# Kernel tuning notes

Measured on AMD Instinct MI355X. Metric: run time of the kernel, lower is better.

The kernel has to match this reference:

```python
import jax, jax.numpy as jnp
import numpy as np

K = 100          # sliding window (even: matches torch pad (K//2, K//2-1) producing T windows)
EPS = 1e-12      # added to std, per original code


def setup_inputs() -> dict:
    key = jax.random.key(0)
    x = jax.random.normal(key, (8, 16384, 128), dtype=jnp.float32)  # B x T x D
    return {"x": x}


def _sliding_mean_std(x):
    """Per-frame sliding mean/std (unbiased, ddof=1) over a reflect-padded
    window of size K, via prefix sums: O(T) instead of O(T*K)."""
    B, T, D = x.shape
    # reflect pad the time axis: left K//2, right K//2-1 -> T + K - 1 frames
    xp = jnp.pad(x, ((0, 0), (K // 2, K // 2 - 1), (0, 0)), mode="reflect")
    zero = jnp.zeros((B, 1, D), dtype=x.dtype)
    cs = jnp.concatenate([zero, jnp.cumsum(xp, axis=1)], axis=1)        # (B, T+K, D)
    cs2 = jnp.concatenate([zero, jnp.cumsum(xp * xp, axis=1)], axis=1)  # (B, T+K, D)
    s = cs[:, K:K + T] - cs[:, 0:T]    # window sums,   (B, T, D)
    s2 = cs2[:, K:K + T] - cs2[:, 0:T]  # window sumsq, (B, T, D)
    m = s / K
    var = (s2 - K * m * m) / (K - 1)    # unbiased variance (torch.std default)
    std = jnp.sqrt(jnp.maximum(var, 0.0))
    return m, std


def reference(x) -> jnp.ndarray:
    # with_mean=True, with_std=True branch of MovingAvgNorm (T >= kernel_size)
    m, std = _sliding_mean_std(x)
    return (x - m) / (std + EPS)
```

## Files before the change

### kernel.cpp

```cpp
#include <hip/hip_runtime.h>

constexpr int KWIN = 100;
constexpr int HK   = 50;
constexpr int TSUB = 64;
constexpr int MB   = 8;
constexpr int PB   = 25;

template <bool REFLECT>
__device__ __forceinline__ int tidx(int t) {
    if constexpr (REFLECT) {
        constexpr int T = 16384;
        t = (t < 0) ? -t : t;
        return (t >= T) ? (2 * T - 2 - t) : t;
    }
    return t;
}

template <bool REFLECT>
__device__ __forceinline__ void run_chunk(
    const float* __restrict__ xb, float* __restrict__ ob, const int t0)
{
    float ring[HK];
    float sx = 0.f, sq = 0.f;

    {
        float la[PB], lb[PB];
        #pragma unroll
        for (int j = 0; j < PB; ++j)
            la[j] = xb[(size_t)tidx<REFLECT>(t0 - HK + j) * 128];
        #pragma unroll
        for (int j = 0; j < PB; ++j)
            lb[j] = xb[(size_t)tidx<REFLECT>(t0 - PB + j) * 128];
        #pragma unroll
        for (int j = 0; j < PB; ++j) { sx += la[j]; sq = fmaf(la[j], la[j], sq); }
        #pragma unroll
        for (int j = 0; j < PB; ++j)
            ring[j] = xb[(size_t)tidx<REFLECT>(t0 + j) * 128];
        #pragma unroll
        for (int j = 0; j < PB; ++j) { sx += lb[j]; sq = fmaf(lb[j], lb[j], sq); }
        #pragma unroll
        for (int j = 0; j < PB; ++j)
            ring[PB + j] = xb[(size_t)tidx<REFLECT>(t0 + PB + j) * 128];
        #pragma unroll
        for (int j = 0; j < PB; ++j) { sx += ring[j]; sq = fmaf(ring[j], ring[j], sq); }
        #pragma unroll
        for (int j = 0; j < PB; ++j) { sx += ring[PB + j]; sq = fmaf(ring[PB + j], ring[PB + j], sq); }
    }

    const float invK   = 1.0f / (float)KWIN;
    const float invKm1 = 1.0f / (float)(KWIN - 1);
    const float fK     = (float)KWIN;

    float inA[MB], outA[MB], inB[MB], outB[MB];

#define LOADB(IN, OUT, KB)                                                    \
    {                                                                         \
        _Pragma("unroll")                                                     \
        for (int j = 0; j < MB; ++j) {                                        \
            const int t = t0 + (KB) + j;                                      \
            IN[j]  = xb[(size_t)tidx<REFLECT>(t + HK) * 128];                 \
            OUT[j] = xb[(size_t)tidx<REFLECT>(t - HK) * 128];                 \
        }                                                                     \
    }

#define COMPUTEB(IN, OUT, KB)                                                 \
    {                                                                         \
        _Pragma("unroll")                                                     \
        for (int j = 0; j < MB; ++j) {                                        \
            const int k = (KB) + j;                                           \
            const float c  = ring[k % HK];                                    \
            const float m  = sx * invK;                                       \
            const float va = fmaxf((sq - fK * m * m) * invKm1, 1e-24f);       \
            const float rs = __builtin_amdgcn_rsqf(va);                       \
            __builtin_nontemporal_store((c - m) * rs,                         \
                                        &ob[(size_t)(t0 + k) * 128]);         \
            sx += IN[j] - OUT[j];                                             \
            sq += IN[j] * IN[j] - OUT[j] * OUT[j];                            \
            ring[k % HK] = IN[j];                                             \
        }                                                                     \
    }

    LOADB(inA, outA, 0 * MB);
    LOADB(inB, outB, 1 * MB);
    COMPUTEB(inA, outA, 0 * MB);
    LOADB(inA, outA, 2 * MB);
    COMPUTEB(inB, outB, 1 * MB);
    LOADB(inB, outB, 3 * MB);
    COMPUTEB(inA, outA, 2 * MB);
    LOADB(inA, outA, 4 * MB);
    COMPUTEB(inB, outB, 3 * MB);
    LOADB(inB, outB, 5 * MB);
    COMPUTEB(inA, outA, 4 * MB);
    LOADB(inA, outA, 6 * MB);
    COMPUTEB(inB, outB, 5 * MB);
    LOADB(inB, outB, 7 * MB);
    COMPUTEB(inA, outA, 6 * MB);
    COMPUTEB(inB, outB, 7 * MB);

#undef LOADB
#undef COMPUTEB
}

__global__ __launch_bounds__(256, 2) void man_kernel(
    const float* __restrict__ x, float* __restrict__ out)
{
    constexpr int T = 16384, D = 128;

    const int i   = blockIdx.x;
    const int bb  = (i & 7) * 128 + (i >> 3);
    const int b   = bb >> 7;
    const int seg = bb & 127;
    const int w   = threadIdx.x >> 7;
    const int tid = threadIdx.x & 127;
    const int t0  = (seg * 2 + w) * TSUB;

    const float* __restrict__ xb = x   + (size_t)b * T * D + tid;
    float*       __restrict__ ob = out + (size_t)b * T * D + tid;

    if (t0 >= HK && t0 + TSUB - 1 + HK < T) {
        run_chunk<false>(xb, ob, t0);
    } else {
        run_chunk<true>(xb, ob, t0);
    }
}

extern "C" void kernel_launch(void* const* d_in, const int* in_sizes, int n_in,
                              void* d_out, int out_size, void* d_ws, size_t ws_size,
                              hipStream_t stream) {
    (void)in_sizes; (void)n_in; (void)d_ws; (void)ws_size; (void)out_size;
    const float* x = (const float*)d_in[0];
    float* out = (float*)d_out;
    man_kernel<<<dim3(1024), dim3(256), 0, stream>>>(x, out);
}
```

Before: 30.00 us.

## Stage normalized output through LDS and write it back as 128-bit vector stores

Each thread now writes its normalized outputs into a double-buffered shared-memory tile covering 16 rows. After a barrier, the tile is flushed to global memory with float4 stores, which cuts the store instruction count by four. The compute batch size drops from 8 to 4, and the reflect-boundary blocks move to a simple scalar path that returns early. In exchange, the kernel adds block barriers and LDS traffic, and it gives up the nontemporal store hint, while global stores were already coalesced before.

```diff
diff --git a/kernel.cpp b/kernel.cpp
--- a/kernel.cpp
+++ b/kernel.cpp
@@ -3,125 +3,146 @@
 constexpr int KWIN = 100;
 constexpr int HK   = 50;
 constexpr int TSUB = 64;
-constexpr int MB   = 8;
+constexpr int MB   = 4;
 constexpr int PB   = 25;
 
-template <bool REFLECT>
-__device__ __forceinline__ int tidx(int t) {
-    if constexpr (REFLECT) {
-        constexpr int T = 16384;
-        t = (t < 0) ? -t : t;
-        return (t >= T) ? (2 * T - 2 - t) : t;
-    }
-    return t;
-}
+typedef float f32x4 __attribute__((ext_vector_type(4)));
 
-template <bool REFLECT>
-__device__ __forceinline__ void run_chunk(
-    const float* __restrict__ xb, float* __restrict__ ob, const int t0)
-{
-    float ring[HK];
-    float sx = 0.f, sq = 0.f;
-
-    {
-        float la[PB], lb[PB];
-        #pragma unroll
-        for (int j = 0; j < PB; ++j)
-            la[j] = xb[(size_t)tidx<REFLECT>(t0 - HK + j) * 128];
-        #pragma unroll
-        for (int j = 0; j < PB; ++j)
-            lb[j] = xb[(size_t)tidx<REFLECT>(t0 - PB + j) * 128];
-        #pragma unroll
-        for (int j = 0; j < PB; ++j) { sx += la[j]; sq = fmaf(la[j], la[j], sq); }
-        #pragma unroll
-        for (int j = 0; j < PB; ++j)
-            ring[j] = xb[(size_t)tidx<REFLECT>(t0 + j) * 128];
-        #pragma unroll
-        for (int j = 0; j < PB; ++j) { sx += lb[j]; sq = fmaf(lb[j], lb[j], sq); }
-        #pragma unroll
-        for (int j = 0; j < PB; ++j)
-            ring[PB + j] = xb[(size_t)tidx<REFLECT>(t0 + PB + j) * 128];
-        #pragma unroll
-        for (int j = 0; j < PB; ++j) { sx += ring[j]; sq = fmaf(ring[j], ring[j], sq); }
-        #pragma unroll
-        for (int j = 0; j < PB; ++j) { sx += ring[PB + j]; sq = fmaf(ring[PB + j], ring[PB + j], sq); }
-    }
-
-    const float invK   = 1.0f / (float)KWIN;
-    const float invKm1 = 1.0f / (float)(KWIN - 1);
-    const float fK     = (float)KWIN;
-
-    float inA[MB], outA[MB], inB[MB], outB[MB];
-
-#define LOADB(IN, OUT, KB)                                                    \
-    {                                                                         \
-        _Pragma("unroll")                                                     \
-        for (int j = 0; j < MB; ++j) {                                        \
-            const int t = t0 + (KB) + j;                                      \
-            IN[j]  = xb[(size_t)tidx<REFLECT>(t + HK) * 128];                 \
-            OUT[j] = xb[(size_t)tidx<REFLECT>(t - HK) * 128];                 \
-        }                                                                     \
-    }
-
-#define COMPUTEB(IN, OUT, KB)                                                 \
-    {                                                                         \
-        _Pragma("unroll")                                                     \
-        for (int j = 0; j < MB; ++j) {                                        \
-            const int k = (KB) + j;                                           \
-            const float c  = ring[k % HK];                                    \
-            const float m  = sx * invK;                                       \
-            const float va = fmaxf((sq - fK * m * m) * invKm1, 1e-24f);       \
-            const float rs = __builtin_amdgcn_rsqf(va);                       \
-            __builtin_nontemporal_store((c - m) * rs,                         \
-                                        &ob[(size_t)(t0 + k) * 128]);         \
-            sx += IN[j] - OUT[j];                                             \
-            sq += IN[j] * IN[j] - OUT[j] * OUT[j];                            \
-            ring[k % HK] = IN[j];                                             \
-        }                                                                     \
-    }
-
-    LOADB(inA, outA, 0 * MB);
-    LOADB(inB, outB, 1 * MB);
-    COMPUTEB(inA, outA, 0 * MB);
-    LOADB(inA, outA, 2 * MB);
-    COMPUTEB(inB, outB, 1 * MB);
-    LOADB(inB, outB, 3 * MB);
-    COMPUTEB(inA, outA, 2 * MB);
-    LOADB(inA, outA, 4 * MB);
-    COMPUTEB(inB, outB, 3 * MB);
-    LOADB(inB, outB, 5 * MB);
-    COMPUTEB(inA, outA, 4 * MB);
-    LOADB(inA, outA, 6 * MB);
-    COMPUTEB(inB, outB, 5 * MB);
-    LOADB(inB, outB, 7 * MB);
-    COMPUTEB(inA, outA, 6 * MB);
-    COMPUTEB(inB, outB, 7 * MB);
-
-#undef LOADB
-#undef COMPUTEB
+__device__ __forceinline__ int ridx(int t) {
+    constexpr int T = 16384;
+    t = (t < 0) ? -t : t;
+    return (t >= T) ? (2 * T - 2 - t) : t;
 }
 
 __global__ __launch_bounds__(256, 2) void man_kernel(
     const float* __restrict__ x, float* __restrict__ out)
 {
     constexpr int T = 16384, D = 128;
+    __shared__ float sbuf[2][2][16 * 128];
 
     const int i   = blockIdx.x;
     const int bb  = (i & 7) * 128 + (i >> 3);
     const int b   = bb >> 7;
     const int seg = bb & 127;
     const int w   = threadIdx.x >> 7;
-    const int tid = threadIdx.x & 127;
+    const int d   = threadIdx.x & 127;
     const int t0  = (seg * 2 + w) * TSUB;
 
-    const float* __restrict__ xb = x   + (size_t)b * T * D + tid;
-    float*       __restrict__ ob = out + (size_t)b * T * D + tid;
+    const float* __restrict__ xb = x + (size_t)b * T * D + d;
+    float* __restrict__ og = out + (size_t)b * T * D + (size_t)t0 * D;
 
-    if (t0 >= HK && t0 + TSUB - 1 + HK < T) {
-        run_chunk<false>(xb, ob, t0);
-    } else {
-        run_chunk<true>(xb, ob, t0);
+    const float invK = 1.0f / 100.0f, invKm1 = 1.0f / 99.0f, fK = 100.0f;
+
+    float ring[HK];
+    float sx = 0.f, sq = 0.f;
+
+    if (seg == 0 || seg == 127) {
+        #pragma unroll
+        for (int s = 0; s < HK; ++s) {
+            float v = xb[(size_t)ridx(t0 - HK + s) * D];
+            sx += v; sq = fmaf(v, v, sq);
+        }
+        #pragma unroll
+        for (int s = 0; s < HK; ++s) {
+            float v = xb[(size_t)ridx(t0 + s) * D];
+            ring[s] = v; sx += v; sq = fmaf(v, v, sq);
+        }
+        #pragma unroll
+        for (int k = 0; k < TSUB; ++k) {
+            float in = xb[(size_t)ridx(t0 + k + HK) * D];
+            float o  = xb[(size_t)ridx(t0 + k - HK) * D];
+            float c  = ring[k % HK];
+            float m  = sx * invK;
+            float va = fmaxf((sq - fK * m * m) * invKm1, 1e-24f);
+            float rs = __builtin_amdgcn_rsqf(va);
+            og[(size_t)k * D + d] = (c - m) * rs;
+            sx += in - o; sq += in * in - o * o;
+            ring[k % HK] = in;
+        }
+        return;
     }
+
+    {
+        float la[PB], lb_[PB];
+        #pragma unroll
+        for (int j = 0; j < PB; ++j) la[j]  = xb[(size_t)(t0 - HK + j) * D];
+        #pragma unroll
+        for (int j = 0; j < PB; ++j) lb_[j] = xb[(size_t)(t0 - PB + j) * D];
+        #pragma unroll
+        for (int j = 0; j < PB; ++j) { sx += la[j]; sq = fmaf(la[j], la[j], sq); }
+        #pragma unroll
+        for (int j = 0; j < PB; ++j) la[j] = xb[(size_t)(t0 + j) * D];
+        #pragma unroll
+        for (int j = 0; j < PB; ++j) { sx += lb_[j]; sq = fmaf(lb_[j], lb_[j], sq); }
+        #pragma unroll
+        for (int j = 0; j < PB; ++j) lb_[j] = xb[(size_t)(t0 + PB + j) * D];
+        #pragma unroll
+        for (int j = 0; j < PB; ++j) { ring[j] = la[j]; sx += la[j]; sq = fmaf(la[j], la[j], sq); }
+        #pragma unroll
+        for (int j = 0; j < PB; ++j) { ring[PB + j] = lb_[j]; sx += lb_[j]; sq = fmaf(lb_[j], lb_[j], sq); }
+    }
+
+    float inA[MB], oA[MB], inB[MB], oB[MB];
+
+#define LOADB(IN, OU, KB)                                                     \
+    {                                                                         \
+        _Pragma("unroll")                                                     \
+        for (int j = 0; j < MB; ++j) {                                        \
+            IN[j] = xb[(size_t)(t0 + (KB) * MB + j + HK) * D];                \
+            OU[j] = xb[(size_t)(t0 + (KB) * MB + j - HK) * D];                \
+        }                                                                     \
+    }
+
+#define COMPUTEB(IN, OU, KB)                                                  \
+    {                                                                         \
+        _Pragma("unroll")                                                     \
+        for (int j = 0; j < MB; ++j) {                                        \
+            const int k = (KB) * MB + j;                                      \
+            const float c  = ring[k % HK];                                    \
+            const float m  = sx * invK;                                       \
+            const float va = fmaxf((sq - fK * m * m) * invKm1, 1e-24f);       \
+            const float rs = __builtin_amdgcn_rsqf(va);                       \
+            sbuf[((KB) / 4) & 1][w][(k % 16) * 128 + d] = (c - m) * rs;       \
+            sx += IN[j] - OU[j];                                              \
+            sq += IN[j] * IN[j] - OU[j] * OU[j];                              \
+            ring[k % HK] = IN[j];                                             \
+        }                                                                     \
+    }
+
+#define FLUSH(G)                                                              \
+    {                                                                         \
+        asm volatile("s_waitcnt lgkmcnt(0)\n\ts_barrier" ::: "memory");       \
+        const float* ls_ = &sbuf[(G) & 1][w][0];                              \
+        _Pragma("unroll")                                                     \
+        for (int p = 0; p < 4; ++p) {                                         \
+            f32x4 v = *(const f32x4*)(ls_ + p * 512 + d * 4);                 \
+            *(f32x4*)(&og[(size_t)((G) * 16 + p * 4 + (d >> 5)) * D           \
+                          + (d & 31) * 4]) = v;                               \
+        }                                                                     \
+    }
+
+    LOADB(inA, oA, 0); LOADB(inB, oB, 1);
+    COMPUTEB(inA, oA, 0);  LOADB(inA, oA, 2);
+    COMPUTEB(inB, oB, 1);  LOADB(inB, oB, 3);
+    COMPUTEB(inA, oA, 2);  LOADB(inA, oA, 4);
+    COMPUTEB(inB, oB, 3);  LOADB(inB, oB, 5);  FLUSH(0);
+    COMPUTEB(inA, oA, 4);  LOADB(inA, oA, 6);
+    COMPUTEB(inB, oB, 5);  LOADB(inB, oB, 7);
+    COMPUTEB(inA, oA, 6);  LOADB(inA, oA, 8);
+    COMPUTEB(inB, oB, 7);  LOADB(inB, oB, 9);  FLUSH(1);
+    COMPUTEB(inA, oA, 8);  LOADB(inA, oA, 10);
+    COMPUTEB(inB, oB, 9);  LOADB(inB, oB, 11);
+    COMPUTEB(inA, oA, 10); LOADB(inA, oA, 12);
+    COMPUTEB(inB, oB, 11); LOADB(inB, oB, 13); FLUSH(2);
+    COMPUTEB(inA, oA, 12); LOADB(inA, oA, 14);
+    COMPUTEB(inB, oB, 13); LOADB(inB, oB, 15);
+    COMPUTEB(inA, oA, 14);
+    COMPUTEB(inB, oB, 15);
+    FLUSH(3);
+
+#undef LOADB
+#undef COMPUTEB
+#undef FLUSH
 }
 
 extern "C" void kernel_launch(void* const* d_in, const int* in_sizes, int n_in,
```

Result: slower. 38.28 us (+27.6%).
